# Kernel tuning notes

Measured on AMD Instinct MI355X. Metric: run time of the kernel, lower is better.

Reference implementation:

```python
import jax, jax.numpy as jnp
import numpy as np

D_MODEL = 1024
NUM_HEADS = 16
HEAD_DIM = D_MODEL // NUM_HEADS


def setup_inputs() -> dict:
    key = jax.random.key(0)
    ks = jax.random.split(key, 11)
    B, S = 4, 2048
    scale = 1.0 / np.sqrt(D_MODEL)
    inp = {
        "k": jax.random.normal(ks[0], (B, S, D_MODEL), jnp.float32),
        "q": jax.random.normal(ks[1], (B, S, D_MODEL), jnp.float32),
        "v": jax.random.normal(ks[2], (B, S, D_MODEL), jnp.float32),
        "w_k": jax.random.normal(ks[3], (D_MODEL, D_MODEL), jnp.float32) * scale,
        "b_k": jnp.zeros((D_MODEL,), jnp.float32),
        "w_q": jax.random.normal(ks[4], (D_MODEL, D_MODEL), jnp.float32) * scale,
        "b_q": jnp.zeros((D_MODEL,), jnp.float32),
        "w_v": jax.random.normal(ks[5], (D_MODEL, D_MODEL), jnp.float32) * scale,
        "b_v": jnp.zeros((D_MODEL,), jnp.float32),
        "w_o": jax.random.normal(ks[6], (D_MODEL, D_MODEL), jnp.float32) * scale,
        "b_o": jnp.zeros((D_MODEL,), jnp.float32),
    }
    return inp


def _split_heads(x):
    B, S, _ = x.shape
    return x.reshape(B, S, NUM_HEADS, HEAD_DIM).transpose(0, 2, 1, 3)  # [B,H,S,Dh]


def reference(k, q, v, w_k, b_k, w_q, b_q, w_v, b_v, w_o, b_o):
    # Linear projections (torch Linear: x @ W.T + b; here weights stored as [in,out])
    kp = k @ w_k + b_k
    qp = q @ w_q + b_q
    vp = v @ w_v + b_v
    kh = _split_heads(kp)
    qh = _split_heads(qp)
    vh = _split_heads(vp)
    # NOTE: original divides by head_dim, not sqrt(head_dim)
    scores = jnp.einsum("bhsd,bhtd->bhst", qh, kh) / HEAD_DIM
    attn = jax.nn.softmax(scores, axis=-1)
    # dropout is identity in eval mode (deterministic baseline)
    ctx = jnp.einsum("bhst,bhtd->bhsd", attn, vh)
    B, H, S, Dh = ctx.shape
    ctx = ctx.transpose(0, 2, 1, 3).reshape(B, S, D_MODEL)
    return ctx @ w_o + b_o
```

## Files before the change

kernel.cpp:

```cpp
#include <hip/hip_runtime.h>

#define D_MODEL 1024
#define S_LEN   2048
#define BATCH   4
#define NHEAD   16
#define HDIM    64
#define NTOK    (BATCH * S_LEN)

typedef __attribute__((ext_vector_type(8))) __bf16 bf16x8;
typedef __attribute__((ext_vector_type(4))) __bf16 bf16x4;
typedef __attribute__((ext_vector_type(4))) float  floatx4;

static __device__ inline floatx4 mfma16(bf16x8 a, bf16x8 b, floatx4 c) {
    return __builtin_amdgcn_mfma_f32_16x16x32_bf16(a, b, c, 0, 0, 0);
}

static __device__ inline void gload_lds16(const __bf16* g, __bf16* l) {
    __builtin_amdgcn_global_load_lds(
        (const __attribute__((address_space(1))) void*)g,
        (__attribute__((address_space(3))) void*)l, 16, 0, 0);
}

#define BARRIER()  asm volatile("s_barrier" ::: "memory")
#define WAITVM4()  asm volatile("s_waitcnt vmcnt(4)" ::: "memory")
#define WAITLGKM() asm volatile("s_waitcnt lgkmcnt(0)" ::: "memory")

__global__ __launch_bounds__(256) void cvt_qkv(const float* __restrict__ k,
                                               const float* __restrict__ q,
                                               const float* __restrict__ v,
                                               __bf16* __restrict__ kb,
                                               __bf16* __restrict__ qb,
                                               __bf16* __restrict__ vb) {
    const float* x = (blockIdx.y == 0) ? k : (blockIdx.y == 1) ? q : v;
    __bf16* y = (blockIdx.y == 0) ? kb : (blockIdx.y == 1) ? qb : vb;
    size_t i = ((size_t)blockIdx.x * 256 + threadIdx.x) * 8;
    float4 a = *(const float4*)(x + i);
    float4 b = *(const float4*)(x + i + 4);
    bf16x8 o;
    o[0] = (__bf16)a.x; o[1] = (__bf16)a.y; o[2] = (__bf16)a.z; o[3] = (__bf16)a.w;
    o[4] = (__bf16)b.x; o[5] = (__bf16)b.y; o[6] = (__bf16)b.z; o[7] = (__bf16)b.w;
    *(bf16x8*)(y + i) = o;
}

__global__ __launch_bounds__(256) void cvt_w4(const float* __restrict__ w0,
                                              const float* __restrict__ w1,
                                              const float* __restrict__ w2,
                                              const float* __restrict__ w3,
                                              __bf16* __restrict__ t0,
                                              __bf16* __restrict__ t1,
                                              __bf16* __restrict__ t2,
                                              __bf16* __restrict__ t3) {
    const int z = blockIdx.z;
    const float* W = (z == 0) ? w0 : (z == 1) ? w1 : (z == 2) ? w2 : w3;
    __bf16* Wt = (z == 0) ? t0 : (z == 1) ? t1 : (z == 2) ? t2 : t3;
    __shared__ __bf16 t[64][72];
    const int i0 = blockIdx.x * 64;
    const int j0 = blockIdx.y * 64;
    const int tid = threadIdx.x;
    const int r4 = tid >> 4, c4 = (tid & 15) * 4;
#pragma unroll
    for (int rr = 0; rr < 64; rr += 16) {
        int r = rr + r4;
        float4 v = *(const float4*)(W + (size_t)(i0 + r) * D_MODEL + j0 + c4);
        t[c4 + 0][r] = (__bf16)v.x;
        t[c4 + 1][r] = (__bf16)v.y;
        t[c4 + 2][r] = (__bf16)v.z;
        t[c4 + 3][r] = (__bf16)v.w;
    }
    __syncthreads();
    const int r8 = tid >> 3, c8 = (tid & 7) * 8;
#pragma unroll
    for (int rr = 0; rr < 64; rr += 32) {
        int r = rr + r8;
        bf16x8 o;
#pragma unroll
        for (int e = 0; e < 8; e++) o[e] = t[r][c8 + e];
        *(bf16x8*)(Wt + (size_t)(j0 + r) * D_MODEL + i0 + c8) = o;
    }
}

#define BM 128
#define BN 128
#define BK 32
template <int OUT_F32>
__device__ __forceinline__ void gemm_body(const __bf16* __restrict__ A,
                                          const __bf16* __restrict__ Bt,
                                          void* __restrict__ Cp,
                                          const float* __restrict__ biasN,
                                          const float* __restrict__ biasM,
                                          int N, int K, float scale,
                                          int bm, int bn,
                                          __bf16* lA, __bf16* lB) {
    const int tid = threadIdx.x;
    const int wave = tid >> 6, lane = tid & 63;
    const int quad = lane >> 4, l16 = lane & 15;
    const int wm = (wave >> 1) * 64, wn = (wave & 1) * 64;
    const int c0 = wave * 128 + lane;

    floatx4 acc[4][4];
#pragma unroll
    for (int i = 0; i < 4; i++)
#pragma unroll
        for (int j = 0; j < 4; j++) acc[i][j] = (floatx4){0.f, 0.f, 0.f, 0.f};

    const __bf16* Ag = A + (size_t)bm * K;
    const __bf16* Bg = Bt + (size_t)bn * K;

    for (int k0 = 0; k0 < K; k0 += BK) {
        __syncthreads();
#pragma unroll
        for (int i = 0; i < 2; i++) {
            int c = c0 + i * 64;
            int row = c >> 2, col = (c & 3) * 8;
            gload_lds16(Ag + (size_t)row * K + k0 + col, lA + c * 8);
            gload_lds16(Bg + (size_t)row * K + k0 + col, lB + c * 8);
        }
        __syncthreads();
        bf16x8 af[4], bf[4];
#pragma unroll
        for (int i = 0; i < 4; i++) {
            af[i] = *(const bf16x8*)(lA + (wm + i * 16 + l16) * BK + quad * 8);
            bf[i] = *(const bf16x8*)(lB + (wn + i * 16 + l16) * BK + quad * 8);
        }
#pragma unroll
        for (int i = 0; i < 4; i++)
#pragma unroll
            for (int j = 0; j < 4; j++) acc[i][j] = mfma16(af[i], bf[j], acc[i][j]);
    }

#pragma unroll
    for (int i = 0; i < 4; i++) {
#pragma unroll
        for (int r = 0; r < 4; r++) {
            int row = bm + wm + i * 16 + quad * 4 + r;
            float brow = biasM ? biasM[row] : 0.0f;
#pragma unroll
            for (int j = 0; j < 4; j++) {
                int col = bn + wn + j * 16 + l16;
                float v = (acc[i][j][r] + brow + (biasN ? biasN[col] : 0.0f)) * scale;
                if constexpr (OUT_F32)
                    ((float*)Cp)[(size_t)row * N + col] = v;
                else
                    ((__bf16*)Cp)[(size_t)row * N + col] = (__bf16)v;
            }
        }
    }
}

__global__ __launch_bounds__(256) void qkv_gemm(const __bf16* __restrict__ kb,
                                                const __bf16* __restrict__ qb,
                                                const __bf16* __restrict__ vb,
                                                const __bf16* __restrict__ WtK,
                                                const __bf16* __restrict__ WtQ,
                                                const __bf16* __restrict__ WtV,
                                                __bf16* Kp, __bf16* Qp, __bf16* Vtp,
                                                const float* b_k, const float* b_q,
                                                const float* b_v, float qscale) {
    __shared__ __bf16 lA[BM * BK];
    __shared__ __bf16 lB[BN * BK];
    const int z = blockIdx.z;
    if (z == 0)
        gemm_body<0>(kb, WtK, Kp, b_k, nullptr, D_MODEL, D_MODEL, 1.0f,
                     blockIdx.x * BM, blockIdx.y * BN, lA, lB);
    else if (z == 1)
        gemm_body<0>(qb, WtQ, Qp, b_q, nullptr, D_MODEL, D_MODEL, qscale,
                     blockIdx.x * BM, blockIdx.y * BN, lA, lB);
    else
        gemm_body<0>(WtV, vb, Vtp, nullptr, b_v, NTOK, D_MODEL, 1.0f,
                     blockIdx.y * BM, blockIdx.x * BN, lA, lB);
}

__global__ __launch_bounds__(256) void out_gemm(const __bf16* __restrict__ A,
                                                const __bf16* __restrict__ Bt,
                                                float* __restrict__ C,
                                                const float* __restrict__ biasN) {
    __shared__ __bf16 lA[BM * BK];
    __shared__ __bf16 lB[BN * BK];
    gemm_body<1>(A, Bt, C, biasN, nullptr, D_MODEL, D_MODEL, 1.0f,
                 blockIdx.x * BM, blockIdx.y * BN, lA, lB);
}

#define QT_M 128
#define KVT  64
__global__ __launch_bounds__(256) void attn(const __bf16* __restrict__ Qp,
                                            const __bf16* __restrict__ Kp,
                                            const __bf16* __restrict__ Vt,
                                            __bf16* __restrict__ ctx) {
    const int qt = blockIdx.x, h = blockIdx.y, b = blockIdx.z;
    const int tid = threadIdx.x;
    const int wave = tid >> 6, lane = tid & 63;
    const int quad = lane >> 4, l16 = lane & 15;
    const int swz = l16 & 7;

    __shared__ __bf16 lK[2][KVT * HDIM];
    __shared__ __bf16 lV[2][HDIM * KVT];
    __shared__ __bf16 lP[4][32 * 64];

    const int qbase = b * S_LEN + qt * QT_M + wave * 32;
    bf16x8 qf[2][2];
#pragma unroll
    for (int m = 0; m < 2; m++)
#pragma unroll
        for (int hf = 0; hf < 2; hf++)
            qf[m][hf] = *(const bf16x8*)(Qp + (size_t)(qbase + m * 16 + l16) * D_MODEL +
                                         h * HDIM + hf * 32 + quad * 8);

    floatx4 octx[2][4];
    floatx4 lsumv[2];
#pragma unroll
    for (int m = 0; m < 2; m++) {
#pragma unroll
        for (int j = 0; j < 4; j++) octx[m][j] = (floatx4){0.f, 0.f, 0.f, 0.f};
        lsumv[m] = (floatx4){0.f, 0.f, 0.f, 0.f};
    }
    bf16x8 ones;
#pragma unroll
    for (int e = 0; e < 8; e++) ones[e] = (__bf16)1.0f;

    const __bf16* Kg = Kp + (size_t)(b * S_LEN) * D_MODEL + h * HDIM;
    const __bf16* Vg = Vt + (size_t)(h * HDIM) * NTOK + (size_t)b * S_LEN;

#pragma unroll
    for (int i = 0; i < 2; i++) {
        int g = i * 256 + tid;
        int row = g >> 3, cl = (g & 7) ^ (row & 7);
        gload_lds16(Kg + (size_t)row * D_MODEL + cl * 8, &lK[0][g * 8]);
        gload_lds16(Vg + (size_t)row * NTOK + cl * 8, &lV[0][g * 8]);
    }

    __bf16* lPw = &lP[wave][0];

    for (int it = 0; it < S_LEN / KVT; ++it) {
        const int cur = it & 1, nxt = cur ^ 1;
        const int t0n = ((it + 1) * KVT) & (S_LEN - 1);

        BARRIER();
#pragma unroll
        for (int i = 0; i < 2; i++) {
            int g = i * 256 + tid;
            int row = g >> 3, cl = (g & 7) ^ (row & 7);
            gload_lds16(Kg + (size_t)(t0n + row) * D_MODEL + cl * 8, &lK[nxt][g * 8]);
            gload_lds16(Vg + (size_t)row * NTOK + t0n + cl * 8, &lV[nxt][g * 8]);
        }
        WAITVM4();
        BARRIER();

        floatx4 sc[2][4];
#pragma unroll
        for (int tt = 0; tt < 4; tt++) {
            sc[0][tt] = (floatx4){0.f, 0.f, 0.f, 0.f};
            sc[1][tt] = (floatx4){0.f, 0.f, 0.f, 0.f};
#pragma unroll
            for (int hf = 0; hf < 2; hf++) {
                bf16x8 kf = *(const bf16x8*)(&lK[cur][(tt * 16 + l16) * HDIM +
                                                      (((hf << 2) | quad) ^ swz) * 8]);
                sc[0][tt] = mfma16(kf, qf[0][hf], sc[0][tt]);
                sc[1][tt] = mfma16(kf, qf[1][hf], sc[1][tt]);
            }
        }

#pragma unroll
        for (int m = 0; m < 2; m++)
#pragma unroll
            for (int tt = 0; tt < 4; tt++) {
                bf16x4 w;
#pragma unroll
                for (int r = 0; r < 4; r++) w[r] = (__bf16)exp2f(sc[m][tt][r]);
                int c = tt * 4 + quad;
                int g = c >> 1, half = c & 1;
                *(bf16x4*)(lPw + (m * 16 + l16) * 64 + ((g ^ swz) * 8 + half * 4)) = w;
            }
        WAITLGKM();

#pragma unroll
        for (int kh = 0; kh < 2; kh++) {
            bf16x8 pf0 = *(const bf16x8*)(lPw + (0 + l16) * 64 +
                                          ((((kh << 2) | quad) ^ swz) * 8));
            bf16x8 pf1 = *(const bf16x8*)(lPw + (16 + l16) * 64 +
                                          ((((kh << 2) | quad) ^ swz) * 8));
            lsumv[0] = mfma16(pf0, ones, lsumv[0]);
            lsumv[1] = mfma16(pf1, ones, lsumv[1]);
#pragma unroll
            for (int j = 0; j < 4; j++) {
                bf16x8 vf = *(const bf16x8*)(&lV[cur][(j * 16 + l16) * KVT +
                                                      (((kh << 2) | quad) ^ swz) * 8]);
                octx[0][j] = mfma16(pf0, vf, octx[0][j]);
                octx[1][j] = mfma16(pf1, vf, octx[1][j]);
            }
        }
    }

#pragma unroll
    for (int m = 0; m < 2; m++)
#pragma unroll
        for (int r = 0; r < 4; r++) {
            float linv = 1.0f / lsumv[m][r];
            int qrow = qbase + m * 16 + quad * 4 + r;
#pragma unroll
            for (int j = 0; j < 4; j++) {
                int col = h * HDIM + j * 16 + l16;
                ctx[(size_t)qrow * D_MODEL + col] = (__bf16)(octx[m][j][r] * linv);
            }
        }
}

extern "C" void kernel_launch(void* const* d_in, const int* in_sizes, int n_in,
                              void* d_out, int out_size, void* d_ws, size_t ws_size,
                              hipStream_t stream) {
    (void)in_sizes; (void)n_in; (void)out_size; (void)ws_size;
    const float* k_in = (const float*)d_in[0];
    const float* q_in = (const float*)d_in[1];
    const float* v_in = (const float*)d_in[2];
    const float* w_k  = (const float*)d_in[3];
    const float* b_k  = (const float*)d_in[4];
    const float* w_q  = (const float*)d_in[5];
    const float* b_q  = (const float*)d_in[6];
    const float* w_v  = (const float*)d_in[7];
    const float* b_v  = (const float*)d_in[8];
    const float* w_o  = (const float*)d_in[9];
    const float* b_o  = (const float*)d_in[10];

    char* ws = (char*)d_ws;
    const size_t SZ = (size_t)NTOK * D_MODEL * sizeof(__bf16);
    __bf16* kb  = (__bf16*)(ws + 0 * SZ);
    __bf16* qb  = (__bf16*)(ws + 1 * SZ);
    __bf16* vb  = (__bf16*)(ws + 2 * SZ);
    __bf16* WtK = (__bf16*)(ws + 3 * SZ);
    __bf16* WtQ = WtK + (size_t)D_MODEL * D_MODEL;
    __bf16* WtV = WtQ + (size_t)D_MODEL * D_MODEL;
    __bf16* WtO = WtV + (size_t)D_MODEL * D_MODEL;
    __bf16* Kp  = (__bf16*)(ws + 3 * SZ + 4 * (size_t)D_MODEL * D_MODEL * sizeof(__bf16));
    __bf16* Qp  = Kp + (size_t)NTOK * D_MODEL;
    __bf16* Vtp = Qp + (size_t)NTOK * D_MODEL;
    __bf16* ctx = kb;

    const float QSCALE = 1.44269504f / 64.0f;

    cvt_qkv<<<dim3(NTOK * D_MODEL / (256 * 8), 3), 256, 0, stream>>>(
        k_in, q_in, v_in, kb, qb, vb);
    cvt_w4<<<dim3(16, 16, 4), 256, 0, stream>>>(w_k, w_q, w_v, w_o, WtK, WtQ, WtV, WtO);

    qkv_gemm<<<dim3(64, 8, 3), 256, 0, stream>>>(kb, qb, vb, WtK, WtQ, WtV,
                                                 Kp, Qp, Vtp, b_k, b_q, b_v, QSCALE);

    attn<<<dim3(S_LEN / QT_M, NHEAD, BATCH), 256, 0, stream>>>(Qp, Kp, Vtp, ctx);

    out_gemm<<<dim3(64, 8), 256, 0, stream>>>(ctx, WtO, (float*)d_out, b_o);
}
```

Baseline: 410.1 us.

## Enlarge attention query tile and compute row sums on VALU with fast exp

Doubles the attention query tile to 256 rows, so each wave handles 64 query rows and each K/V tile loaded into LDS is reused across twice as many queries. Row sums are now accumulated in floats on the vector ALU and reduced with cross-lane shuffles, replacing the MFMA-against-ones trick. The loop is unrolled by two with compile-time buffer indices, exp uses the hardware exp2 builtin, and bf16 packing is done with bit operations. The cost is higher register and LDS pressure (larger P buffer, launch_bounds of 2 blocks) and half as many blocks in the grid. The rounding in pack_bf16 adds 0x8000 and truncates, which can differ from round-to-nearest-even in tie cases.

Result: faster. 358.2 us (-12.7%).

```diff
diff --git a/kernel.cpp b/kernel.cpp
--- a/kernel.cpp
+++ b/kernel.cpp
@@ -8,7 +8,6 @@
 #define NTOK    (BATCH * S_LEN)
 
 typedef __attribute__((ext_vector_type(8))) __bf16 bf16x8;
-typedef __attribute__((ext_vector_type(4))) __bf16 bf16x4;
 typedef __attribute__((ext_vector_type(4))) float  floatx4;
 
 static __device__ inline floatx4 mfma16(bf16x8 a, bf16x8 b, floatx4 c) {
@@ -24,6 +23,22 @@
 #define BARRIER()  asm volatile("s_barrier" ::: "memory")
 #define WAITVM4()  asm volatile("s_waitcnt vmcnt(4)" ::: "memory")
 #define WAITLGKM() asm volatile("s_waitcnt lgkmcnt(0)" ::: "memory")
+
+#if __has_builtin(__builtin_amdgcn_exp2f)
+#define EXP2(x) __builtin_amdgcn_exp2f(x)
+#else
+#define EXP2(x) exp2f(x)
+#endif
+
+static __device__ inline unsigned pack_bf16(float a, float b) {
+    unsigned ua = __builtin_bit_cast(unsigned, a) + 0x8000u;
+    unsigned ub = __builtin_bit_cast(unsigned, b) + 0x8000u;
+#if __has_builtin(__builtin_amdgcn_perm)
+    return __builtin_amdgcn_perm(ub, ua, 0x07060302u);
+#else
+    return (ua >> 16) | (ub & 0xffff0000u);
+#endif
+}
 
 __global__ __launch_bounds__(256) void cvt_qkv(const float* __restrict__ k,
                                                const float* __restrict__ q,
@@ -180,12 +195,74 @@
                  blockIdx.x * BM, blockIdx.y * BN, lA, lB);
 }
 
-#define QT_M 128
+#define QT_M 256
 #define KVT  64
-__global__ __launch_bounds__(256) void attn(const __bf16* __restrict__ Qp,
-                                            const __bf16* __restrict__ Kp,
-                                            const __bf16* __restrict__ Vt,
-                                            __bf16* __restrict__ ctx) {
+
+template <int CUR>
+__device__ __forceinline__ void attn_step(
+    __bf16 (&lK)[2][KVT * HDIM], __bf16 (&lV)[2][HDIM * KVT], __bf16* lPw,
+    const __bf16* Kg, const __bf16* Vg, int t0n,
+    const bf16x8 (&qf)[4][2], floatx4 (&octx)[4][4], float (&lsum)[4],
+    int tid, int quad, int l16, int swz) {
+    constexpr int NXT = CUR ^ 1;
+
+    BARRIER();
+#pragma unroll
+    for (int i = 0; i < 2; i++) {
+        int g = i * 256 + tid;
+        int row = g >> 3, cl = (g & 7) ^ (row & 7);
+        gload_lds16(Kg + (size_t)(t0n + row) * D_MODEL + cl * 8, &lK[NXT][g * 8]);
+        gload_lds16(Vg + (size_t)row * NTOK + t0n + cl * 8, &lV[NXT][g * 8]);
+    }
+    WAITVM4();
+    BARRIER();
+
+#pragma unroll
+    for (int tt = 0; tt < 4; tt++) {
+        bf16x8 kf0 = *(const bf16x8*)(&lK[CUR][(tt * 16 + l16) * HDIM + ((0 + quad) ^ swz) * 8]);
+        bf16x8 kf1 = *(const bf16x8*)(&lK[CUR][(tt * 16 + l16) * HDIM + ((4 + quad) ^ swz) * 8]);
+        floatx4 sc[4];
+#pragma unroll
+        for (int m = 0; m < 4; m++) {
+            sc[m] = mfma16(kf0, qf[m][0], (floatx4){0.f, 0.f, 0.f, 0.f});
+            sc[m] = mfma16(kf1, qf[m][1], sc[m]);
+        }
+        int c = tt * 4 + quad;
+        int g = c >> 1, half = c & 1;
+        int off = ((g ^ swz) * 8 + half * 4);
+#pragma unroll
+        for (int m = 0; m < 4; m++) {
+            float p0 = EXP2(sc[m][0]), p1 = EXP2(sc[m][1]);
+            float p2 = EXP2(sc[m][2]), p3 = EXP2(sc[m][3]);
+            lsum[m] += (p0 + p1) + (p2 + p3);
+            unsigned lo = pack_bf16(p0, p1), hi = pack_bf16(p2, p3);
+            *(uint2*)(lPw + (m * 16 + l16) * 64 + off) = make_uint2(lo, hi);
+        }
+    }
+    WAITLGKM();
+
+#pragma unroll
+    for (int kh = 0; kh < 2; kh++) {
+        int goff = (((kh << 2) | quad) ^ swz) * 8;
+        bf16x8 vf[4], pf[4];
+#pragma unroll
+        for (int j = 0; j < 4; j++)
+            vf[j] = *(const bf16x8*)(&lV[CUR][(j * 16 + l16) * KVT + goff]);
+#pragma unroll
+        for (int m = 0; m < 4; m++)
+            pf[m] = *(const bf16x8*)(lPw + (m * 16 + l16) * 64 + goff);
+#pragma unroll
+        for (int m = 0; m < 4; m++)
+#pragma unroll
+            for (int j = 0; j < 4; j++)
+                octx[m][j] = mfma16(pf[m], vf[j], octx[m][j]);
+    }
+}
+
+__global__ __launch_bounds__(256, 2) void attn(const __bf16* __restrict__ Qp,
+                                               const __bf16* __restrict__ Kp,
+                                               const __bf16* __restrict__ Vt,
+                                               __bf16* __restrict__ ctx) {
     const int qt = blockIdx.x, h = blockIdx.y, b = blockIdx.z;
     const int tid = threadIdx.x;
     const int wave = tid >> 6, lane = tid & 63;
@@ -194,28 +271,25 @@
 
     __shared__ __bf16 lK[2][KVT * HDIM];
     __shared__ __bf16 lV[2][HDIM * KVT];
-    __shared__ __bf16 lP[4][32 * 64];
-
-    const int qbase = b * S_LEN + qt * QT_M + wave * 32;
-    bf16x8 qf[2][2];
-#pragma unroll
-    for (int m = 0; m < 2; m++)
+    __shared__ __bf16 lP[4][64 * 64];
+
+    const int qbase = b * S_LEN + qt * QT_M + wave * 64;
+    bf16x8 qf[4][2];
+#pragma unroll
+    for (int m = 0; m < 4; m++)
 #pragma unroll
         for (int hf = 0; hf < 2; hf++)
             qf[m][hf] = *(const bf16x8*)(Qp + (size_t)(qbase + m * 16 + l16) * D_MODEL +
                                          h * HDIM + hf * 32 + quad * 8);
 
-    floatx4 octx[2][4];
-    floatx4 lsumv[2];
-#pragma unroll
-    for (int m = 0; m < 2; m++) {
+    floatx4 octx[4][4];
+    float lsum[4];
+#pragma unroll
+    for (int m = 0; m < 4; m++) {
 #pragma unroll
         for (int j = 0; j < 4; j++) octx[m][j] = (floatx4){0.f, 0.f, 0.f, 0.f};
-        lsumv[m] = (floatx4){0.f, 0.f, 0.f, 0.f};
-    }
-    bf16x8 ones;
-#pragma unroll
-    for (int e = 0; e < 8; e++) ones[e] = (__bf16)1.0f;
+        lsum[m] = 0.f;
+    }
 
     const __bf16* Kg = Kp + (size_t)(b * S_LEN) * D_MODEL + h * HDIM;
     const __bf16* Vg = Vt + (size_t)(h * HDIM) * NTOK + (size_t)b * S_LEN;
@@ -230,71 +304,21 @@
 
     __bf16* lPw = &lP[wave][0];
 
-    for (int it = 0; it < S_LEN / KVT; ++it) {
-        const int cur = it & 1, nxt = cur ^ 1;
-        const int t0n = ((it + 1) * KVT) & (S_LEN - 1);
-
-        BARRIER();
-#pragma unroll
-        for (int i = 0; i < 2; i++) {
-            int g = i * 256 + tid;
-            int row = g >> 3, cl = (g & 7) ^ (row & 7);
-            gload_lds16(Kg + (size_t)(t0n + row) * D_MODEL + cl * 8, &lK[nxt][g * 8]);
-            gload_lds16(Vg + (size_t)row * NTOK + t0n + cl * 8, &lV[nxt][g * 8]);
-        }
-        WAITVM4();
-        BARRIER();
-
-        floatx4 sc[2][4];
-#pragma unroll
-        for (int tt = 0; tt < 4; tt++) {
-            sc[0][tt] = (floatx4){0.f, 0.f, 0.f, 0.f};
-            sc[1][tt] = (floatx4){0.f, 0.f, 0.f, 0.f};
-#pragma unroll
-            for (int hf = 0; hf < 2; hf++) {
-                bf16x8 kf = *(const bf16x8*)(&lK[cur][(tt * 16 + l16) * HDIM +
-                                                      (((hf << 2) | quad) ^ swz) * 8]);
-                sc[0][tt] = mfma16(kf, qf[0][hf], sc[0][tt]);
-                sc[1][tt] = mfma16(kf, qf[1][hf], sc[1][tt]);
-            }
-        }
-
-#pragma unroll
-        for (int m = 0; m < 2; m++)
-#pragma unroll
-            for (int tt = 0; tt < 4; tt++) {
-                bf16x4 w;
-#pragma unroll
-                for (int r = 0; r < 4; r++) w[r] = (__bf16)exp2f(sc[m][tt][r]);
-                int c = tt * 4 + quad;
-                int g = c >> 1, half = c & 1;
-                *(bf16x4*)(lPw + (m * 16 + l16) * 64 + ((g ^ swz) * 8 + half * 4)) = w;
-            }
-        WAITLGKM();
-
-#pragma unroll
-        for (int kh = 0; kh < 2; kh++) {
-            bf16x8 pf0 = *(const bf16x8*)(lPw + (0 + l16) * 64 +
-                                          ((((kh << 2) | quad) ^ swz) * 8));
-            bf16x8 pf1 = *(const bf16x8*)(lPw + (16 + l16) * 64 +
-                                          ((((kh << 2) | quad) ^ swz) * 8));
-            lsumv[0] = mfma16(pf0, ones, lsumv[0]);
-            lsumv[1] = mfma16(pf1, ones, lsumv[1]);
-#pragma unroll
-            for (int j = 0; j < 4; j++) {
-                bf16x8 vf = *(const bf16x8*)(&lV[cur][(j * 16 + l16) * KVT +
-                                                      (((kh << 2) | quad) ^ swz) * 8]);
-                octx[0][j] = mfma16(pf0, vf, octx[0][j]);
-                octx[1][j] = mfma16(pf1, vf, octx[1][j]);
-            }
-        }
-    }
-
-#pragma unroll
-    for (int m = 0; m < 2; m++)
+    for (int it2 = 0; it2 < S_LEN / KVT / 2; ++it2) {
+        attn_step<0>(lK, lV, lPw, Kg, Vg, (2 * it2 + 1) * KVT,
+                     qf, octx, lsum, tid, quad, l16, swz);
+        attn_step<1>(lK, lV, lPw, Kg, Vg, ((2 * it2 + 2) * KVT) & (S_LEN - 1),
+                     qf, octx, lsum, tid, quad, l16, swz);
+    }
+
+#pragma unroll
+    for (int m = 0; m < 4; m++) {
+        float l = lsum[m];
+        l += __shfl_xor(l, 16, 64);
+        l += __shfl_xor(l, 32, 64);
 #pragma unroll
         for (int r = 0; r < 4; r++) {
-            float linv = 1.0f / lsumv[m][r];
+            float linv = 1.0f / __shfl(l, quad * 4 + r, 64);
             int qrow = qbase + m * 16 + quad * 4 + r;
 #pragma unroll
             for (int j = 0; j < 4; j++) {
@@ -302,6 +326,7 @@
                 ctx[(size_t)qrow * D_MODEL + col] = (__bf16)(octx[m][j][r] * linv);
             }
         }
+    }
 }
 
 extern "C" void kernel_launch(void* const* d_in, const int* in_sizes, int n_in,
```
